# Kernel optimization log

Measured on AMD Instinct MI355X. Metric: run time of the kernel, lower is better.

The kernel has to match this reference:

```python
import jax, jax.numpy as jnp
import numpy as np

B, T = 4, 2048
OBS, ST = 512, 512
H, E = 8, 64

def setup_inputs() -> dict:
    key = jax.random.key(0)
    k1, k2, k3, k4, k5 = jax.random.split(key, 5)
    observe = jax.random.normal(k1, (B, T, OBS), dtype=jnp.float32)
    state = jax.random.normal(k2, (B, T, ST), dtype=jnp.float32)
    # nn.Linear weights (out, in) applied as x @ W.T; store transposed for einsum
    Wq = jax.random.normal(k3, (OBS, H * E), dtype=jnp.float32) * (1.0 / np.sqrt(OBS))
    Wk = jax.random.normal(k4, (ST, H * E), dtype=jnp.float32) * (1.0 / np.sqrt(ST))
    Wv = jax.random.normal(k5, (ST, H * E), dtype=jnp.float32) * (1.0 / np.sqrt(ST))
    merge_w = jnp.ones((1, H, E), dtype=jnp.float32)  # Merger weight, init fill_(1.0)
    return {"observe": observe, "state": state, "Wq": Wq, "Wk": Wk, "Wv": Wv, "merge_w": merge_w}

def reference(observe, state, Wq, Wk, Wv, merge_w):
    b, t, _ = observe.shape
    h, e = H, E
    scale = e ** 0.25
    q = (observe @ Wq).reshape(b, t, h, e).transpose(0, 2, 1, 3) / scale  # [b,h,t,e]
    k = (state @ Wk).reshape(b, t, h, e).transpose(0, 2, 1, 3) / scale
    v = (state @ Wv).reshape(b, t, h, e).transpose(0, 2, 1, 3)
    dot = jnp.einsum('bhqe,bhke->bhqk', q, k)  # [b,h,t,t]
    attn = jax.nn.softmax(dot, axis=-1)
    out = jnp.einsum('bhqk,bhke->bhqe', attn, v)  # [b,h,t,e]
    out = out.transpose(0, 2, 1, 3).reshape(b * t, h, e)  # [b*t,h,e]
    # Merger: softmax over head dim of learned weight, weighted head sum
    w = jax.nn.softmax(merge_w, axis=1)  # [1,h,e]
    return jnp.sum(w * out, axis=1)  # [b*t,e]
```

## Files before the change

### kernel.cpp

```cpp
#include <hip/hip_runtime.h>

#define B_ 4
#define T_ 2048
#define H_ 8
#define E_ 64
#define KDIM 512

typedef unsigned short ushort_t;
typedef __attribute__((ext_vector_type(4))) float f32x4;
typedef __attribute__((ext_vector_type(4))) int i32x4;
typedef __attribute__((ext_vector_type(8))) short s16x8;

#define QK_SCALE 0.42466043f

__device__ __forceinline__ ushort_t f2bf(float f) {
  unsigned u = __builtin_bit_cast(unsigned, f);
  u += 0x7fffu + ((u >> 16) & 1u);
  return (ushort_t)(u >> 16);
}
__device__ __forceinline__ unsigned pk2(float a, float b) {
  return (unsigned)f2bf(a) | ((unsigned)f2bf(b) << 16);
}
__device__ __forceinline__ unsigned pk2t(float a, float b) {
  return __builtin_amdgcn_perm(__builtin_bit_cast(unsigned, b),
                               __builtin_bit_cast(unsigned, a), 0x07060302u);
}
__device__ __forceinline__ float e2(float x) { return __builtin_amdgcn_exp2f(x); }
__device__ __forceinline__ void gl2lds16(const void* g, void* l) {
  __builtin_amdgcn_global_load_lds((const __attribute__((address_space(1))) unsigned*)g,
                                   (__attribute__((address_space(3))) unsigned*)l, 16, 0, 0);
}

__global__ void k_prep(const float* __restrict__ Wq, const float* __restrict__ Wk,
                       const float* __restrict__ Wv, ushort_t* __restrict__ wt) {
  __shared__ ushort_t tile[64][66];
  int z = blockIdx.z;
  const float* W = (z == 0) ? Wq : (z == 1 ? Wk : Wv);
  float scale = (z < 2) ? QK_SCALE : 1.0f;
  int k0 = blockIdx.y << 6, n0 = blockIdx.x << 6;
  int rr = threadIdx.x >> 6, cc = threadIdx.x & 63;
  for (int p = 0; p < 16; p++) {
    int kl = p * 4 + rr;
    tile[cc][kl] = f2bf(W[(size_t)(k0 + kl) * 512 + n0 + cc] * scale);
  }
  __syncthreads();
  int kp2 = threadIdx.x & 31, nr = threadIdx.x >> 5;
  unsigned* wt32 = (unsigned*)(wt + (size_t)z * 262144);
  for (int p = 0; p < 8; p++) {
    int nl = p * 8 + nr;
    unsigned val = (unsigned)tile[nl][kp2 * 2] | ((unsigned)tile[nl][kp2 * 2 + 1] << 16);
    wt32[(size_t)(n0 + nl) * 256 + (k0 >> 1) + kp2] = val;
  }
}

__global__ void k_wgt(const float* __restrict__ mw, float* __restrict__ wgt) {
  int e = threadIdx.x;
  float w[8], wmax = -1e30f;
  for (int h = 0; h < 8; h++) { w[h] = mw[h * 64 + e]; wmax = fmaxf(wmax, w[h]); }
  float wsum = 0.f;
  for (int h = 0; h < 8; h++) { w[h] = __expf(w[h] - wmax); wsum += w[h]; }
  float inv = 1.f / wsum;
  for (int h = 0; h < 8; h++) wgt[h * 64 + e] = w[h] * inv;
}

__global__ void k_cvt(const float* __restrict__ obs, const float* __restrict__ st,
                      unsigned* __restrict__ xo, unsigned* __restrict__ xs) {
  int which = blockIdx.y;
  const float* src = which ? st : obs;
  unsigned* dst = which ? xs : xo;
  size_t idx = (size_t)blockIdx.x * 256 + threadIdx.x;
  size_t base = idx * 8;
  float4 x0 = *(const float4*)(src + base);
  float4 x1 = *(const float4*)(src + base + 4);
  uint4 d;
  d.x = pk2(x0.x, x0.y);
  d.y = pk2(x0.z, x0.w);
  d.z = pk2(x1.x, x1.y);
  d.w = pk2(x1.z, x1.w);
  *(uint4*)(dst + idx * 4) = d;
}

__global__ __launch_bounds__(256, 3) void k_proj2(
    const ushort_t* __restrict__ xo, const ushort_t* __restrict__ xs,
    const ushort_t* __restrict__ wt,
    ushort_t* __restrict__ qo, ushort_t* __restrict__ ko, ushort_t* __restrict__ vto) {
  __shared__ __align__(16) ushort_t As[3][128 * 64];

  int id = blockIdx.x;
  int xcd = id & 7, nt = (id >> 3) & 3, ghi = id >> 5;
  int g = ghi * 8 + xcd;
  int which = g >> 6, mb = g & 63;
  int m0 = mb << 7, n0 = nt << 7;
  const ushort_t* X = (which == 0) ? xo : xs;
  const ushort_t* W = wt + which * 262144;

  int tid = threadIdx.x, wave = tid >> 6, lane = tid & 63;
  int l15 = lane & 15, quad = lane >> 4;
  int wm = wave & 1, wn = wave >> 1;

  f32x4 acc[4][4];
  for (int i = 0; i < 4; i++)
    for (int j = 0; j < 4; j++) acc[i][j] = (f32x4){0.f, 0.f, 0.f, 0.f};

  int arl = lane >> 3, ap = lane & 7;

#define STAGEA(buf, k0)                                                            \
  do {                                                                             \
    for (int ii = 0; ii < 4; ii++) {                                               \
      int r = wave * 32 + ii * 8 + arl;                                            \
      gl2lds16(X + (size_t)(m0 + r) * KDIM + (k0) + ((ap ^ (r & 7)) << 3),         \
               &As[buf][(wave * 32 + ii * 8) * 64]);                               \
    }                                                                              \
  } while (0)

  const ushort_t* wb[4];
  for (int j = 0; j < 4; j++)
    wb[j] = W + (size_t)(n0 + wn * 64 + j * 16 + l15) * KDIM + quad * 8;

  STAGEA(0, 0);
  STAGEA(1, 64);
  __builtin_amdgcn_s_waitcnt(0x0F74);
  __builtin_amdgcn_s_barrier();
  __builtin_amdgcn_sched_barrier(0);

#pragma unroll
  for (int kt = 0; kt < 8; kt++) {
    s16x8 b[2][4];
    for (int kc = 0; kc < 2; kc++)
      for (int j = 0; j < 4; j++) b[kc][j] = *(const s16x8*)(wb[j] + kc * 32);
    for (int j = 0; j < 4; j++) wb[j] += 64;
    if (kt < 6) STAGEA((kt + 2) % 3, (kt + 2) * 64);
    if (kt < 6) __builtin_amdgcn_s_waitcnt(0x0F74);
    else        __builtin_amdgcn_s_waitcnt(0x0F70);
    __builtin_amdgcn_sched_barrier(0);
    const ushort_t* asb = As[kt % 3];
    for (int kc = 0; kc < 2; kc++) {
      s16x8 a[4];
      for (int i = 0; i < 4; i++) {
        int mr = wm * 64 + i * 16 + l15;
        int pc = (kc * 4 + quad) ^ (l15 & 7);
        a[i] = *(const s16x8*)&asb[mr * 64 + pc * 8];
      }
      if (which == 2) {
        for (int i = 0; i < 4; i++)
          for (int j = 0; j < 4; j++)
            acc[i][j] = __builtin_amdgcn_mfma_f32_16x16x32_bf16(b[kc][j], a[i], acc[i][j], 0, 0, 0);
      } else {
        for (int i = 0; i < 4; i++)
          for (int j = 0; j < 4; j++)
            acc[i][j] = __builtin_amdgcn_mfma_f32_16x16x32_bf16(a[i], b[kc][j], acc[i][j], 0, 0, 0);
      }
    }
    if (kt < 7) {
      __builtin_amdgcn_s_barrier();
      __builtin_amdgcn_sched_barrier(0);
    }
  }
#undef STAGEA

  if (which != 2) {
    ushort_t* dst = (which == 0) ? qo : ko;
    for (int i = 0; i < 4; i++) {
      int grow = m0 + wm * 64 + i * 16 + quad * 4;
      for (int j = 0; j < 4; j++) {
        int gcol = n0 + wn * 64 + j * 16 + l15;
        int h = gcol >> 6, e = gcol & 63;
        for (int r = 0; r < 4; r++) {
          int row = grow + r;
          int bb = row >> 11, t = row & 2047;
          int bh = bb * H_ + h;
          dst[(((size_t)bh * T_ + t) << 6) + e] = f2bf(acc[i][j][r]);
        }
      }
    }
  } else {
    for (int i = 0; i < 4; i++) {
      int row = m0 + wm * 64 + i * 16 + l15;
      int bb = row >> 11, t = row & 2047;
      for (int j = 0; j < 4; j++) {
        for (int r = 0; r < 4; r++) {
          int gcol = n0 + wn * 64 + j * 16 + quad * 4 + r;
          int h = gcol >> 6, e = gcol & 63;
          int bh = bb * H_ + h;
          vto[((size_t)(bh << 6) + e) * T_ + t] = f2bf(acc[i][j][r]);
        }
      }
    }
  }
}

__global__ __launch_bounds__(256, 3) void k_proj(
    const float* __restrict__ obs, const float* __restrict__ st,
    const ushort_t* __restrict__ wt,
    ushort_t* __restrict__ qo, ushort_t* __restrict__ ko, ushort_t* __restrict__ vto) {
  __shared__ __align__(16) float As[2][128 * 32];

  int id = blockIdx.x;
  int xcd = id & 7, nt = (id >> 3) & 3, ghi = id >> 5;
  int g = ghi * 8 + xcd;
  int which = g >> 6, mb = g & 63;
  int m0 = mb << 7, n0 = nt << 7;
  const float* X = (which == 0) ? obs : st;
  const ushort_t* W = wt + which * 262144;

  int tid = threadIdx.x, wave = tid >> 6, lane = tid & 63;
  int l15 = lane & 15, quad = lane >> 4;
  int wm = wave & 1, wn = wave >> 1;

  f32x4 acc[4][4];
  for (int i = 0; i < 4; i++)
    for (int j = 0; j < 4; j++) acc[i][j] = (f32x4){0.f, 0.f, 0.f, 0.f};

  int arl = lane >> 3, ap = lane & 7;

#define STAGEA(buf, k0)                                                           \
  do {                                                                            \
    for (int ii = 0; ii < 4; ii++) {                                              \
      int r = wave * 32 + ii * 8 + arl;                                           \
      gl2lds16(X + (size_t)(m0 + r) * KDIM + (k0) + ((ap ^ (r & 7)) << 2),        \
               &As[buf][(wave * 32 + ii * 8) * 32]);                              \
    }                                                                             \
  } while (0)

  const ushort_t* wb[4];
  for (int j = 0; j < 4; j++)
    wb[j] = W + (size_t)(n0 + wn * 64 + j * 16 + l15) * KDIM + quad * 8;

  STAGEA(0, 0);
  __builtin_amdgcn_s_waitcnt(0x0F70);
  __syncthreads();

  for (int kt = 0; kt < 16; kt++) {
    s16x8 b[4];
    for (int j = 0; j < 4; j++) { b[j] = *(const s16x8*)wb[j]; wb[j] += 32; }
    if (kt < 15) STAGEA((kt + 1) & 1, kt * 32 + 32);
    const float* asb = As[kt & 1];
    s16x8 a[4];
    for (int i = 0; i < 4; i++) {
      int mr = wm * 64 + i * 16 + l15;
      int s = mr & 7;
      const float* rowp = &asb[mr * 32];
      float4 x0 = *(const float4*)&rowp[(((quad << 1)) ^ s) << 2];
      float4 x1 = *(const float4*)&rowp[(((quad << 1) | 1) ^ s) << 2];
      i32x4 d;
      d[0] = (int)pk2(x0.x, x0.y);
      d[1] = (int)pk2(x0.z, x0.w);
      d[2] = (int)pk2(x1.x, x1.y);
      d[3] = (int)pk2(x1.z, x1.w);
      a[i] = __builtin_bit_cast(s16x8, d);
    }
    if (which == 2) {
      for (int i = 0; i < 4; i++)
        for (int j = 0; j < 4; j++)
          acc[i][j] = __builtin_amdgcn_mfma_f32_16x16x32_bf16(b[j], a[i], acc[i][j], 0, 0, 0);
    } else {
      for (int i = 0; i < 4; i++)
        for (int j = 0; j < 4; j++)
          acc[i][j] = __builtin_amdgcn_mfma_f32_16x16x32_bf16(a[i], b[j], acc[i][j], 0, 0, 0);
    }
    __builtin_amdgcn_s_waitcnt(0x0F70);
    __syncthreads();
  }
#undef STAGEA

  if (which != 2) {
    ushort_t* dst = (which == 0) ? qo : ko;
    for (int i = 0; i < 4; i++) {
      int grow = m0 + wm * 64 + i * 16 + quad * 4;
      for (int j = 0; j < 4; j++) {
        int gcol = n0 + wn * 64 + j * 16 + l15;
        int h = gcol >> 6, e = gcol & 63;
        for (int r = 0; r < 4; r++) {
          int row = grow + r;
          int bb = row >> 11, t = row & 2047;
          int bh = bb * H_ + h;
          dst[(((size_t)bh * T_ + t) << 6) + e] = f2bf(acc[i][j][r]);
        }
      }
    }
  } else {
    for (int i = 0; i < 4; i++) {
      int row = m0 + wm * 64 + i * 16 + l15;
      int bb = row >> 11, t = row & 2047;
      for (int j = 0; j < 4; j++) {
        for (int r = 0; r < 4; r++) {
          int gcol = n0 + wn * 64 + j * 16 + quad * 4 + r;
          int h = gcol >> 6, e = gcol & 63;
          int bh = bb * H_ + h;
          vto[((size_t)(bh << 6) + e) * T_ + t] = f2bf(acc[i][j][r]);
        }
      }
    }
  }
}

union AttnSmem {
  struct { ushort_t ks[3][64 * 64]; ushort_t vs[3][64 * 64]; } st;
  struct { float ows[64 * 65]; float linv[64]; } ep;
};

__global__ __launch_bounds__(256, 3) void k_attn(
    const ushort_t* __restrict__ q, const ushort_t* __restrict__ k,
    const ushort_t* __restrict__ vt, const float* __restrict__ wgt,
    float* __restrict__ out) {
  __shared__ __align__(16) AttnSmem sm;

  int id = blockIdx.x;
  int bh = id & 31, qt = id >> 5;
  int tid = threadIdx.x, wave = tid >> 6, lane = tid & 63;
  int l15 = lane & 15, quad = lane >> 4;

  s16x8 qf[2];
  {
    const ushort_t* qp =
        q + (((size_t)bh * T_ + qt * 64 + wave * 16 + l15) << 6) + quad * 8;
    qf[0] = *(const s16x8*)qp;
    qf[1] = *(const s16x8*)(qp + 32);
  }
  int hh = bh & 7;
  float wgl = wgt[hh * 64 + lane];

  f32x4 o[4];
  for (int j = 0; j < 4; j++) o[j] = (f32x4){0.f, 0.f, 0.f, 0.f};
  f32x4 lacc = (f32x4){0.f, 0.f, 0.f, 0.f};
  const s16x8 ones = {16256, 16256, 16256, 16256, 16256, 16256, 16256, 16256};

  int srl = lane >> 3, sp = lane & 7;
  const ushort_t* kbase = k + ((size_t)bh * T_ << 6);
  const ushort_t* vbase = vt + ((size_t)bh << 6) * T_;
  const ushort_t* kptr[2];
  const ushort_t* vptr[2];
  for (int ii = 0; ii < 2; ii++) {
    int r = wave * 16 + ii * 8 + srl;
    int gkey = (r & 32) + (((r >> 2) & 3) << 3) + (((r >> 4) & 1) << 2) + (r & 3);
    kptr[ii] = kbase + ((size_t)gkey << 6) + ((sp ^ (r & 7)) << 3);
    int e = r;
    vptr[ii] = vbase + (size_t)e * T_ + ((sp ^ (e & 7)) << 3);
  }

#define STAGE(buf)                                                         \
  do {                                                                     \
    for (int ii = 0; ii < 2; ii++) {                                       \
      gl2lds16(kptr[ii], &sm.st.ks[buf][(wave * 16 + ii * 8) * 64]);       \
      gl2lds16(vptr[ii], &sm.st.vs[buf][(wave * 16 + ii * 8) * 64]);       \
      kptr[ii] += 64 * 64;                                                 \
      vptr[ii] += 64;                                                      \
    }                                                                      \
  } while (0)

  STAGE(0);
  STAGE(1);
  __builtin_amdgcn_s_waitcnt(0x0F74);
  __builtin_amdgcn_s_barrier();
  __builtin_amdgcn_sched_barrier(0);

  int cur = 0, pre = 2;
  for (int kt = 0; kt < 32; kt++) {
    if (kt < 30) STAGE(pre);
    const ushort_t* ksb = &sm.st.ks[0][0] + cur * 4096;
    const ushort_t* vsb = &sm.st.vs[0][0] + cur * 4096;

    __builtin_amdgcn_s_setprio(1);
    s16x8 bfr[2];
    for (int c = 0; c < 2; c++) {
      f32x4 s0 = (f32x4){0.f, 0.f, 0.f, 0.f};
      f32x4 s1 = (f32x4){0.f, 0.f, 0.f, 0.f};
      for (int kc = 0; kc < 2; kc++) {
        int pc = (kc * 4 + quad) ^ (l15 & 7);
        s16x8 k0f = *(const s16x8*)&ksb[(c * 32 + l15) * 64 + pc * 8];
        s16x8 k1f = *(const s16x8*)&ksb[(c * 32 + 16 + l15) * 64 + pc * 8];
        s0 = __builtin_amdgcn_mfma_f32_16x16x32_bf16(k0f, qf[kc], s0, 0, 0, 0);
        s1 = __builtin_amdgcn_mfma_f32_16x16x32_bf16(k1f, qf[kc], s1, 0, 0, 0);
      }
      i32x4 d;
      d[0] = (int)pk2t(e2(s0[0]), e2(s0[1]));
      d[1] = (int)pk2t(e2(s0[2]), e2(s0[3]));
      d[2] = (int)pk2t(e2(s1[0]), e2(s1[1]));
      d[3] = (int)pk2t(e2(s1[2]), e2(s1[3]));
      bfr[c] = __builtin_bit_cast(s16x8, d);
    }

    for (int c = 0; c < 2; c++) {
      lacc = __builtin_amdgcn_mfma_f32_16x16x32_bf16(ones, bfr[c], lacc, 0, 0, 0);
      for (int et = 0; et < 4; et++) {
        int pc = (c * 4 + quad) ^ (l15 & 7);
        s16x8 vf = *(const s16x8*)&vsb[(et * 16 + l15) * 64 + pc * 8];
        o[et] = __builtin_amdgcn_mfma_f32_16x16x32_bf16(vf, bfr[c], o[et], 0, 0, 0);
      }
    }
    __builtin_amdgcn_s_setprio(0);

    if (kt < 30)       __builtin_amdgcn_s_waitcnt(0x0F74);
    else if (kt == 30) __builtin_amdgcn_s_waitcnt(0x0F70);
    if (kt < 31) {
      __builtin_amdgcn_s_barrier();
      __builtin_amdgcn_sched_barrier(0);
    }
    int nc = cur + 1; cur = (nc == 3) ? 0 : nc;
    int np = pre + 1; pre = (np == 3) ? 0 : np;
  }
#undef STAGE

  int bb = bh >> 3;
  __syncthreads();
  {
    int row0 = wave * 16;
    if (quad == 0) sm.ep.linv[row0 + l15] = 1.f / lacc[0];
    for (int et = 0; et < 4; et++)
      for (int r = 0; r < 4; r++)
        sm.ep.ows[(row0 + l15) * 65 + et * 16 + quad * 4 + r] = o[et][r];
    for (int i = 0; i < 16; i++) {
      int row = row0 + i;
      int gt = qt * 64 + row;
      float val = sm.ep.ows[row * 65 + lane] * sm.ep.linv[row] * wgl;
      atomicAdd(&out[(((size_t)bb * T_ + gt) << 6) + lane], val);
    }
  }
}

extern "C" void kernel_launch(void* const* d_in, const int* in_sizes, int n_in,
                              void* d_out, int out_size, void* d_ws, size_t ws_size,
                              hipStream_t stream) {
  const float* obs = (const float*)d_in[0];
  const float* st  = (const float*)d_in[1];
  const float* Wq  = (const float*)d_in[2];
  const float* Wk  = (const float*)d_in[3];
  const float* Wv  = (const float*)d_in[4];
  const float* mw  = (const float*)d_in[5];

  const size_t WS_NEEDED = 27262976;
  const size_t WS_BIG    = 44040192;
  char* ws = (char*)d_ws;
  ushort_t* wt  = (ushort_t*)ws;
  float*    wgt = (float*)(ws + 1572864u);
  ushort_t* qo  = (ushort_t*)(ws + 2097152u);
  ushort_t* ko  = (ushort_t*)(ws + 10485760u);
  ushort_t* vto = (ushort_t*)(ws + 18874368u);
  ushort_t* xo  = (ushort_t*)(ws + 27262976u);
  ushort_t* xs  = (ushort_t*)(ws + 35651584u);
  float*    out = (float*)d_out;

  hipMemsetAsync(d_out, 0, (size_t)out_size * sizeof(float), stream);
  if (ws_size < WS_NEEDED) return;

  hipLaunchKernelGGL(k_prep, dim3(8, 8, 3), dim3(256), 0, stream, Wq, Wk, Wv, wt);
  hipLaunchKernelGGL(k_wgt,  dim3(1),       dim3(64),  0, stream, mw, wgt);
  if (ws_size >= WS_BIG) {
    hipLaunchKernelGGL(k_cvt,   dim3(2048, 2), dim3(256), 0, stream, obs, st,
                       (unsigned*)xo, (unsigned*)xs);
    hipLaunchKernelGGL(k_proj2, dim3(768),     dim3(256), 0, stream, xo, xs, wt, qo, ko, vto);
  } else {
    hipLaunchKernelGGL(k_proj,  dim3(768),     dim3(256), 0, stream, obs, st, wt, qo, ko, vto);
  }
  hipLaunchKernelGGL(k_attn, dim3(1024), dim3(256), 0, stream, qo, ko, vto, wgt, out);
}
```

Baseline: 191.7 us.

## Switch attention K/V staging to double buffer and raise occupancy; reorder projection stores

The attention kernel's K/V LDS staging drops from a 3-deep ring to a 2-deep double buffer, cutting shared memory per block so launch bounds can ask for 4 blocks per CU instead of 3. The prefetch distance shrinks to one tile, and each iteration now waits for all outstanding loads before the barrier, so less load latency is hidden per block in exchange for more resident waves. The projection kernel's epilogue store loops are also reordered so address bases are computed once per row or column rather than per element.

```diff
diff --git a/kernel.cpp b/kernel.cpp
--- a/kernel.cpp
+++ b/kernel.cpp
@@ -160,29 +160,27 @@
 
   if (which != 2) {
     ushort_t* dst = (which == 0) ? qo : ko;
+    int h = (n0 >> 6) + wn;
     for (int i = 0; i < 4; i++) {
-      int grow = m0 + wm * 64 + i * 16 + quad * 4;
-      for (int j = 0; j < 4; j++) {
-        int gcol = n0 + wn * 64 + j * 16 + l15;
+      for (int r = 0; r < 4; r++) {
+        int row = m0 + wm * 64 + i * 16 + quad * 4 + r;
+        int bb = row >> 11, t = row & 2047;
+        size_t lbase = (((size_t)(bb * H_ + h) * T_ + t) << 6);
+        for (int j = 0; j < 4; j++) {
+          int e = ((n0 + wn * 64 + j * 16) & 63) + l15;
+          dst[lbase + e] = f2bf(acc[i][j][r]);
+        }
+      }
+    }
+  } else {
+    for (int j = 0; j < 4; j++) {
+      for (int r = 0; r < 4; r++) {
+        int gcol = n0 + wn * 64 + j * 16 + quad * 4 + r;
         int h = gcol >> 6, e = gcol & 63;
-        for (int r = 0; r < 4; r++) {
-          int row = grow + r;
-          int bb = row >> 11, t = row & 2047;
-          int bh = bb * H_ + h;
-          dst[(((size_t)bh * T_ + t) << 6) + e] = f2bf(acc[i][j][r]);
-        }
-      }
-    }
-  } else {
-    for (int i = 0; i < 4; i++) {
-      int row = m0 + wm * 64 + i * 16 + l15;
-      int bb = row >> 11, t = row & 2047;
-      for (int j = 0; j < 4; j++) {
-        for (int r = 0; r < 4; r++) {
-          int gcol = n0 + wn * 64 + j * 16 + quad * 4 + r;
-          int h = gcol >> 6, e = gcol & 63;
-          int bh = bb * H_ + h;
-          vto[((size_t)(bh << 6) + e) * T_ + t] = f2bf(acc[i][j][r]);
+        size_t lbase = ((size_t)(((m0 >> 11) * H_ + h) << 6) + e) * T_;
+        for (int i = 0; i < 4; i++) {
+          int t = (m0 & 2047) + wm * 64 + i * 16 + l15;
+          vto[lbase + t] = f2bf(acc[i][j][r]);
         }
       }
     }
@@ -295,11 +293,11 @@
 }
 
 union AttnSmem {
-  struct { ushort_t ks[3][64 * 64]; ushort_t vs[3][64 * 64]; } st;
+  struct { ushort_t ks[2][64 * 64]; ushort_t vs[2][64 * 64]; } st;
   struct { float ows[64 * 65]; float linv[64]; } ep;
 };
 
-__global__ __launch_bounds__(256, 3) void k_attn(
+__global__ __launch_bounds__(256, 4) void k_attn(
     const ushort_t* __restrict__ q, const ushort_t* __restrict__ k,
     const ushort_t* __restrict__ vt, const float* __restrict__ wgt,
     float* __restrict__ out) {
@@ -349,16 +347,14 @@
   } while (0)
 
   STAGE(0);
-  STAGE(1);
-  __builtin_amdgcn_s_waitcnt(0x0F74);
+  __builtin_amdgcn_s_waitcnt(0x0F70);
   __builtin_amdgcn_s_barrier();
   __builtin_amdgcn_sched_barrier(0);
 
-  int cur = 0, pre = 2;
   for (int kt = 0; kt < 32; kt++) {
-    if (kt < 30) STAGE(pre);
-    const ushort_t* ksb = &sm.st.ks[0][0] + cur * 4096;
-    const ushort_t* vsb = &sm.st.vs[0][0] + cur * 4096;
+    if (kt < 31) STAGE((kt + 1) & 1);
+    const ushort_t* ksb = &sm.st.ks[0][0] + (kt & 1) * 4096;
+    const ushort_t* vsb = &sm.st.vs[0][0] + (kt & 1) * 4096;
 
     __builtin_amdgcn_s_setprio(1);
     s16x8 bfr[2];
@@ -390,14 +386,11 @@
     }
     __builtin_amdgcn_s_setprio(0);
 
-    if (kt < 30)       __builtin_amdgcn_s_waitcnt(0x0F74);
-    else if (kt == 30) __builtin_amdgcn_s_waitcnt(0x0F70);
     if (kt < 31) {
+      __builtin_amdgcn_s_waitcnt(0x0F70);
       __builtin_amdgcn_s_barrier();
       __builtin_amdgcn_sched_barrier(0);
     }
-    int nc = cur + 1; cur = (nc == 3) ? 0 : nc;
-    int np = pre + 1; pre = (np == 3) ? 0 : np;
   }
 #undef STAGE
 
```

Result: faster. 186.7 us (-2.6%).
